# Kernel tuning notes

Measured on AMD Instinct MI355X. Metric: run time of the kernel, lower is better.

## Reference

```python
import jax, jax.numpy as jnp
import numpy as np

B, S, D, V = 2, 4096, 2048, 32000
H, HD = 16, 128          # heads, head dim (H*HD == D)
BS = 16                  # block_size
N_ANCH = 128             # num_anchors (static: loss_mask=ones guarantees enough valid positions)
MASK_ID = 31999
DFF = 8192


def rms(x, w, eps=1e-6):
    return x * jax.lax.rsqrt(jnp.mean(x * x, axis=-1, keepdims=True) + eps) * w


def rope(x, pos):
    # x: (..., L, H, hd), pos: (..., L)
    hd = x.shape[-1]
    inv = 1.0 / (10000.0 ** (jnp.arange(0, hd, 2, dtype=jnp.float32) / hd))
    ang = pos[..., None, None].astype(jnp.float32) * inv  # (..., L, 1, hd/2)
    cos, sin = jnp.cos(ang), jnp.sin(ang)
    x1, x2 = x[..., : hd // 2], x[..., hd // 2 :]
    return jnp.concatenate([x1 * cos - x2 * sin, x2 * cos + x1 * sin], axis=-1).astype(x.dtype)


def setup_inputs() -> dict:
    key = jax.random.key(0)
    ks = jax.random.split(key, 12)
    s = 0.02
    return {
        "input_ids": jax.random.randint(ks[0], (B, S), 0, V, dtype=jnp.int32),
        "hidden_states": jax.random.normal(ks[1], (B, S, D), dtype=jnp.float32),
        "loss_mask": jnp.ones((B, S), dtype=jnp.float32),
        "rand_vals": jax.random.uniform(ks[2], (B, S - BS + 1), dtype=jnp.float32),
        "embed_table": jax.random.normal(ks[3], (V, D), dtype=jnp.float32) * s,
        "lm_head_w": jax.random.normal(ks[4], (V, D), dtype=jnp.float32) * s,
        "wq": jax.random.normal(ks[5], (D, D), dtype=jnp.float32) * s,
        "wk": jax.random.normal(ks[6], (D, D), dtype=jnp.float32) * s,
        "wv": jax.random.normal(ks[7], (D, D), dtype=jnp.float32) * s,
        "wo": jax.random.normal(ks[8], (D, D), dtype=jnp.float32) * s,
        "w_gate": jax.random.normal(ks[9], (D, DFF), dtype=jnp.float32) * s,
        "w_up": jax.random.normal(ks[10], (D, DFF), dtype=jnp.float32) * s,
        "w_down": jax.random.normal(ks[11], (DFF, D), dtype=jnp.float32) * s,
        "norm_attn": jnp.ones((D,), dtype=jnp.float32),
        "norm_mlp": jnp.ones((D,), dtype=jnp.float32),
        "norm_out": jnp.ones((D,), dtype=jnp.float32),
        "norm_chs": jnp.ones((D,), dtype=jnp.float32),
    }


def reference(input_ids, hidden_states, loss_mask, rand_vals, embed_table, lm_head_w,
              wq, wk, wv, wo, w_gate, w_up, w_down, norm_attn, norm_mlp, norm_out, norm_chs):
    max_anchor = S - BS
    # ---- anchor sampling: random permutation of valid positions via argsort of rand ----
    valid = loss_mask[:, : max_anchor + 1] > 0.5                       # (B, max_anchor+1)
    valid_counts = valid.sum(axis=1)
    idx = jnp.arange(max_anchor + 1, dtype=jnp.int32)
    masked_idx = jnp.where(valid, idx[None, :], S + 1)
    rv = jnp.where(valid, rand_vals, 2.0)
    order = jnp.argsort(rv, axis=1)
    gathered = jnp.take_along_axis(masked_idx, order, axis=1)
    anchors = jnp.sort(gathered[:, :N_ANCH], axis=1)                   # (B, N)
    keep = jnp.arange(N_ANCH)[None, :] < jnp.minimum(valid_counts, N_ANCH)[:, None]
    anchors = jnp.where(keep, anchors, 0)
    # ---- noise embedding: anchor token at block start, mask token elsewhere ----
    anchor_tok = jnp.take_along_axis(input_ids, jnp.clip(anchors, 0, S - 1), axis=1)
    first_tok = jnp.where(keep, anchor_tok, MASK_ID)
    noise_ids = jnp.full((B, N_ANCH, BS), MASK_ID, dtype=jnp.int32).at[:, :, 0].set(first_tok)
    x = embed_table[noise_ids]                                         # (B,N,BS,D)
    # ---- CHS context hidden: target hidden at anchor-1 ----
    ctx_pos = jnp.maximum(anchors - 1, 0)
    ctx = jnp.take_along_axis(hidden_states, ctx_pos[:, :, None], axis=1)  # (B,N,D)
    # ---- block-diagonal attention: per-block kv = [CHS_i | draft block i] (kv_len=1+BS) ----
    pos_q = anchors[:, :, None] + jnp.arange(BS)[None, None, :]        # (B,N,BS)
    pos_kv = jnp.concatenate([ctx_pos[:, :, None], pos_q], axis=2)     # (B,N,1+BS)
    hq = rms(x, norm_attn)
    hc = rms(ctx, norm_chs)[:, :, None, :]
    kv_in = jnp.concatenate([hc, hq], axis=2)                          # (B,N,1+BS,D)
    q = rope((hq @ wq).reshape(B, N_ANCH, BS, H, HD), pos_q)
    k = rope((kv_in @ wk).reshape(B, N_ANCH, 1 + BS, H, HD), pos_kv)
    v = (kv_in @ wv).reshape(B, N_ANCH, 1 + BS, H, HD)
    scores = jnp.einsum('bnqhd,bnkhd->bnhqk', q, k) * (1.0 / HD ** 0.5)
    attn = jax.nn.softmax(scores, axis=-1)
    out = jnp.einsum('bnhqk,bnkhd->bnqhd', attn, v).reshape(B, N_ANCH, BS, D) @ wo
    out = out * keep[:, :, None, None].astype(out.dtype)               # invalid blocks fully masked
    x = x + out
    h = rms(x, norm_mlp)
    x = x + (jax.nn.silu(h @ w_gate) * (h @ w_up)) @ w_down
    h_out = rms(x, norm_out)
    logits = h_out @ lm_head_w.T                                       # (B,N,BS,V)
    # ---- block-wise CE loss ----
    label_idx = anchors[:, :, None] + jnp.arange(BS)[None, None, :]
    valid_label = label_idx < S
    safe = jnp.minimum(label_idx, S - 1)
    targets = jnp.take_along_axis(jnp.broadcast_to(input_ids[:, None, :], (B, N_ANCH, S)), safe, axis=2)
    lm_g = jnp.take_along_axis(jnp.broadcast_to(loss_mask[:, None, :], (B, N_ANCH, S)), safe, axis=2)
    weight = (keep[:, :, None] & valid_label).astype(jnp.float32)
    weight = weight * (jnp.arange(BS) > 0)[None, None, :].astype(jnp.float32) * lm_g
    logp = jax.nn.log_softmax(logits, axis=-1)
    tok_logp = jnp.take_along_axis(logp, targets[..., None].astype(jnp.int32), axis=-1)[..., 0]
    loss = -(tok_logp * weight).sum() / (weight.sum() + 1e-6)
    pred = jnp.argmax(logits, axis=-1)
    accuracy = ((pred == targets) & (weight > 0.5)).sum().astype(jnp.float32) / (weight.sum() + 1e-6)
    return loss, accuracy
```

## Files before the change

### kernel.cpp

```cpp
#include <hip/hip_runtime.h>
#include <math.h>

typedef unsigned short u16;
typedef short v8s __attribute__((ext_vector_type(8)));
typedef u16   v4u __attribute__((ext_vector_type(4)));
typedef float v4f __attribute__((ext_vector_type(4)));

#define DEVFN static __device__ __forceinline__

constexpr int cB = 2, cS = 4096, cD = 2048, cV = 32000, cH = 16, cHD = 128;
constexpr int cBS = 16, cNA = 128, cMASK = 31999, cDFF = 8192;
constexpr int NCAND = cS - cBS + 1;
constexpr int MTOK  = cB * cNA * cBS;
constexpr int MKV   = cB * cNA * 17;
constexpr int NCH   = cV / 128;
constexpr int NCH2  = cV / 256;

constexpr int EPI_BF16 = 0, EPI_SILU = 1, EPI_OEMB = 2, EPI_DOWNACC = 3, EPI_STATS = 4;
constexpr int ASRC_BF16 = 0, ASRC_RMS = 1, ASRC_AOMAP = 2;

struct RmsSrc {
  const float* hs; const float* emb; const float* nattn; const float* nchs;
  const float* rowinv; const int* ftok; const int* cpos;
};

DEVFN u16 f2bf(float f) {
  union { float f; unsigned u; } a; a.f = f;
  unsigned u = a.u;
  u = u + 0x7fffu + ((u >> 16) & 1u);
  return (u16)(u >> 16);
}
DEVFN float bf2f(u16 h) {
  union { unsigned u; float f; } a; a.u = ((unsigned)h) << 16;
  return a.f;
}
DEVFN float waveSum(float v) {
  #pragma unroll
  for (int o = 32; o >= 1; o >>= 1) v += __shfl_xor(v, o);
  return v;
}
DEVFN void gload16(void* lds, const void* g) {
  __builtin_amdgcn_global_load_lds(
      (const __attribute__((address_space(1))) unsigned*)g,
      (__attribute__((address_space(3))) unsigned*)lds, 16, 0, 0);
}

__global__ void k_select(const float* __restrict__ lmask, const float* __restrict__ rv_in,
                         int* __restrict__ self) {
  int b = blockIdx.x >> 4, chunk = blockIdx.x & 15;
  __shared__ float rvs[4096];
  for (int i = threadIdx.x; i < NCAND; i += 256) {
    bool valid = lmask[(size_t)b * cS + i] > 0.5f;
    rvs[i] = valid ? rv_in[(size_t)b * NCAND + i] : 2.0f;
  }
  __syncthreads();
  int i = chunk * 256 + threadIdx.x;
  if (i < NCAND) {
    float v = rvs[i];
    int rank = 0;
    for (int j = 0; j < NCAND; ++j) {
      float u = rvs[j];
      rank += (u < v) || (u == v && j < i);
    }
    self[(size_t)b * NCAND + i] = (rank < cNA) ? 1 : 0;
  }
}

__global__ void k_anchors(const float* __restrict__ lmask, const int* __restrict__ self,
                          const int* __restrict__ ids, int* __restrict__ anchors,
                          int* __restrict__ keepA, int* __restrict__ ftok, int* __restrict__ cpos) {
  int b = blockIdx.x;
  __shared__ int flags[4096];
  __shared__ int ssum[256];
  __shared__ int soff[257];
  __shared__ int abuf[cNA];
  for (int i = threadIdx.x; i < 4096; i += 256)
    flags[i] = (i < NCAND) ? (self[(size_t)b * NCAND + i] && (lmask[(size_t)b * cS + i] > 0.5f)) : 0;
  if (threadIdx.x < cNA) abuf[threadIdx.x] = 0;
  __syncthreads();
  int s = 0;
  #pragma unroll
  for (int j = 0; j < 16; ++j) s += flags[threadIdx.x * 16 + j];
  ssum[threadIdx.x] = s;
  __syncthreads();
  if (threadIdx.x == 0) {
    int a = 0;
    for (int t = 0; t < 256; ++t) { soff[t] = a; a += ssum[t]; }
    soff[256] = a;
  }
  __syncthreads();
  int nsel = soff[256];
  int p = soff[threadIdx.x];
  for (int j = 0; j < 16; ++j) {
    int i = threadIdx.x * 16 + j;
    if (flags[i]) { if (p < cNA) abuf[p] = i; ++p; }
  }
  __syncthreads();
  if (threadIdx.x < cNA) {
    int q = threadIdx.x;
    int kp = (q < nsel) ? 1 : 0;
    int a = kp ? abuf[q] : 0;
    anchors[b * cNA + q] = a;
    keepA[b * cNA + q] = kp;
    int av = a; if (av < 0) av = 0; if (av > cS - 1) av = cS - 1;
    int tok = ids[(size_t)b * cS + av];
    ftok[b * cNA + q] = kp ? tok : cMASK;
    cpos[b * cNA + q] = (a - 1 > 0) ? (a - 1) : 0;
  }
}

__global__ void k_rowinv(const float* __restrict__ hs, const float* __restrict__ emb,
                         const int* __restrict__ ftok, const int* __restrict__ cpos,
                         float* __restrict__ rowinv) {
  int r = blockIdx.x;
  int j = r % 17, bn = r / 17, b = bn >> 7;
  const float* src = (j == 0) ? hs + ((size_t)b * cS + cpos[bn]) * cD
                              : emb + (size_t)((j == 1) ? ftok[bn] : cMASK) * cD;
  float ss = 0.f;
  for (int d = threadIdx.x; d < cD; d += 256) { float v = src[d]; ss += v * v; }
  ss = waveSum(ss);
  __shared__ float red[4];
  if ((threadIdx.x & 63) == 0) red[threadIdx.x >> 6] = ss;
  __syncthreads();
  if (threadIdx.x == 0) {
    float tot = red[0] + red[1] + red[2] + red[3];
    rowinv[r] = 1.0f / sqrtf(tot / cD + 1e-6f);
  }
}

__global__ void k_build2(const float* __restrict__ hs, const float* __restrict__ emb,
                         const float* __restrict__ nattn, const float* __restrict__ nchs,
                         const int* __restrict__ ftok, const int* __restrict__ cpos,
                         u16* __restrict__ kv) {
  int r = blockIdx.x;
  int j = r % 17, bn = r / 17, b = bn >> 7;
  const float* src; const float* w;
  if (j == 0) { src = hs + ((size_t)b * cS + cpos[bn]) * cD; w = nchs; }
  else {
    int tok = (j == 1) ? ftok[bn] : cMASK;
    src = emb + (size_t)tok * cD; w = nattn;
  }
  float ss = 0.f;
  for (int d = threadIdx.x; d < cD; d += 256) { float v = src[d]; ss += v * v; }
  ss = waveSum(ss);
  __shared__ float red[4];
  if ((threadIdx.x & 63) == 0) red[threadIdx.x >> 6] = ss;
  __syncthreads();
  float tot = red[0] + red[1] + red[2] + red[3];
  float inv = 1.0f / sqrtf(tot / cD + 1e-6f);
  for (int d = threadIdx.x; d < cD; d += 256)
    kv[(size_t)r * cD + d] = f2bf(src[d] * inv * w[d]);
}

__global__ void k_rms(const float* __restrict__ xin, const float* __restrict__ w,
                      u16* __restrict__ outp) {
  int m = blockIdx.x;
  const float* row = xin + (size_t)m * cD;
  float ss = 0.f;
  for (int d = threadIdx.x; d < cD; d += 256) { float v = row[d]; ss += v * v; }
  ss = waveSum(ss);
  __shared__ float red[4];
  if ((threadIdx.x & 63) == 0) red[threadIdx.x >> 6] = ss;
  __syncthreads();
  float tot = red[0] + red[1] + red[2] + red[3];
  float inv = 1.0f / sqrtf(tot / cD + 1e-6f);
  for (int d = threadIdx.x; d < cD; d += 256)
    outp[(size_t)m * cD + d] = f2bf(row[d] * inv * w[d]);
}

__global__ void k_conv(const float* __restrict__ in, u16* __restrict__ out, long n) {
  long i = ((long)blockIdx.x * 256 + threadIdx.x) * 8;
  long stride = (long)gridDim.x * 256 * 8;
  for (; i < n; i += stride) {
    v4f a = *(const v4f*)(in + i), b = *(const v4f*)(in + i + 4);
    v8s pk;
    #pragma unroll
    for (int e = 0; e < 4; ++e) { pk[e] = (short)f2bf(a[e]); pk[4 + e] = (short)f2bf(b[e]); }
    *(v8s*)(out + i) = pk;
  }
}

__global__ void k_tconv(const float* __restrict__ W, u16* __restrict__ WT, int K, int N) {
  __shared__ u16 t[64][72];
  int n0 = blockIdx.x * 64, k0 = blockIdx.y * 64;
  int tid = threadIdx.x;
  int c4 = (tid & 15) * 4, r0 = tid >> 4;
  #pragma unroll
  for (int rr = 0; rr < 64; rr += 16) {
    int k = r0 + rr;
    v4f v = *(const v4f*)(W + (size_t)(k0 + k) * N + n0 + c4);
    #pragma unroll
    for (int e = 0; e < 4; ++e) t[c4 + e][k] = f2bf(v[e]);
  }
  __syncthreads();
  int n = tid >> 2, kq = (tid & 3) * 16;
  v8s o0, o1;
  #pragma unroll
  for (int e = 0; e < 8; ++e) { o0[e] = (short)t[n][kq + e]; o1[e] = (short)t[n][kq + 8 + e]; }
  *(v8s*)(WT + (size_t)(n0 + n) * K + k0 + kq) = o0;
  *(v8s*)(WT + (size_t)(n0 + n) * K + k0 + kq + 8) = o1;
}

template <int EPI>
__launch_bounds__(512, 1)
__global__ void k_gemm6(const u16* __restrict__ Abf, const u16* __restrict__ Bbf,
                        u16* __restrict__ Cbf, const u16* __restrict__ Gaux,
                        v4f* __restrict__ partials, int K, int ldc, int nch) {
  __shared__ __align__(16) u16 lds[65536];
  const int tid = threadIdx.x;
  const int lane = tid & 63, wid = tid >> 6;
  const int wm = wid >> 2, wn = wid & 3;
  const int lc = lane & 15, lq = lane >> 4;
  const int m0 = blockIdx.x * 256, n0 = blockIdx.y * 256;

  const u16* srcA[2]; const u16* srcB[2];
  #pragma unroll
  for (int i = 0; i < 2; ++i) {
    int s = i * 512 + tid;
    int row = s >> 2;
    int c2 = (s & 3) ^ ((row >> 1) & 3);
    srcA[i] = Abf + (size_t)(m0 + row) * K + c2 * 8;
    srcB[i] = Bbf + (size_t)(n0 + row) * K + c2 * 8;
  }

  v4f acc[8][4];
  #pragma unroll
  for (int i = 0; i < 8; ++i)
    #pragma unroll
    for (int j = 0; j < 4; ++j) acc[i][j] = (v4f){0.f, 0.f, 0.f, 0.f};

  const int fsw = lq ^ ((lc >> 1) & 3);
  int aoff[8], boff[4];
  #pragma unroll
  for (int mi = 0; mi < 8; ++mi) aoff[mi] = ((wm * 128 + mi * 16 + lc) * 4 + fsw) * 8;
  #pragma unroll
  for (int ni = 0; ni < 4; ++ni) boff[ni] = ((wn * 64 + ni * 16 + lc) * 4 + fsw) * 8;

  auto stageA = [&](int t, int kh) {
    int reg = (t & 1) * 32768 + kh * 8192;
    int koff = t * 64 + kh * 32;
    #pragma unroll
    for (int i = 0; i < 2; ++i)
      gload16(&lds[reg + i * 4096 + wid * 512], srcA[i] + koff);
  };
  auto stageB = [&](int t, int kh) {
    int reg = (t & 1) * 32768 + 16384 + kh * 8192;
    int koff = t * 64 + kh * 32;
    #pragma unroll
    for (int i = 0; i < 2; ++i)
      gload16(&lds[reg + i * 4096 + wid * 512], srcB[i] + koff);
  };

  stageA(0, 0); stageB(0, 0);
  stageA(0, 1); stageB(0, 1);
  stageA(1, 0); stageB(1, 0);
  asm volatile("s_waitcnt vmcnt(8)" ::: "memory");
  __builtin_amdgcn_s_barrier();

  const int NT = K >> 6;
  for (int t = 0; t < NT; ++t) {
    const int bufb = (t & 1) * 32768;
    const u16* Ab0 = &lds[bufb];
    const u16* Ab1 = &lds[bufb + 8192];
    const u16* Bb0 = &lds[bufb + 16384];
    const u16* Bb1 = &lds[bufb + 24576];
    v8s a_[4], b_[4];

    #pragma unroll
    for (int ni = 0; ni < 4; ++ni) b_[ni] = *(const v8s*)(Bb0 + boff[ni]);
    #pragma unroll
    for (int mi = 0; mi < 4; ++mi) a_[mi] = *(const v8s*)(Ab0 + aoff[mi]);
    if (t + 1 < NT) stageA(t + 1, 1);
    asm volatile("s_waitcnt lgkmcnt(0)" ::: "memory");
    __builtin_amdgcn_sched_barrier(0);
    __builtin_amdgcn_s_setprio(1);
    #pragma unroll
    for (int mi = 0; mi < 4; ++mi)
      #pragma unroll
      for (int ni = 0; ni < 4; ++ni)
        acc[mi][ni] = __builtin_amdgcn_mfma_f32_16x16x32_bf16(a_[mi], b_[ni], acc[mi][ni], 0, 0, 0);
    __builtin_amdgcn_s_setprio(0);
    __builtin_amdgcn_s_barrier();

    #pragma unroll
    for (int mi = 0; mi < 4; ++mi) a_[mi] = *(const v8s*)(Ab0 + aoff[mi + 4]);
    if (t + 1 < NT) stageB(t + 1, 1);
    asm volatile("s_waitcnt lgkmcnt(0)" ::: "memory");
    __builtin_amdgcn_sched_barrier(0);
    __builtin_amdgcn_s_setprio(1);
    #pragma unroll
    for (int mi = 0; mi < 4; ++mi)
      #pragma unroll
      for (int ni = 0; ni < 4; ++ni)
        acc[mi + 4][ni] = __builtin_amdgcn_mfma_f32_16x16x32_bf16(a_[mi], b_[ni], acc[mi + 4][ni], 0, 0, 0);
    __builtin_amdgcn_s_setprio(0);
    if (t + 1 < NT) { asm volatile("s_waitcnt vmcnt(4)" ::: "memory"); }
    else            { asm volatile("s_waitcnt vmcnt(0)" ::: "memory"); }
    __builtin_amdgcn_s_barrier();

    #pragma unroll
    for (int ni = 0; ni < 4; ++ni) b_[ni] = *(const v8s*)(Bb1 + boff[ni]);
    #pragma unroll
    for (int mi = 0; mi < 4; ++mi) a_[mi] = *(const v8s*)(Ab1 + aoff[mi]);
    if (t + 2 < NT) stageA(t + 2, 0);
    asm volatile("s_waitcnt lgkmcnt(0)" ::: "memory");
    __builtin_amdgcn_sched_barrier(0);
    __builtin_amdgcn_s_setprio(1);
    #pragma unroll
    for (int mi = 0; mi < 4; ++mi)
      #pragma unroll
      for (int ni = 0; ni < 4; ++ni)
        acc[mi][ni] = __builtin_amdgcn_mfma_f32_16x16x32_bf16(a_[mi], b_[ni], acc[mi][ni], 0, 0, 0);
    __builtin_amdgcn_s_setprio(0);
    __builtin_amdgcn_s_barrier();

    #pragma unroll
    for (int mi = 0; mi < 4; ++mi) a_[mi] = *(const v8s*)(Ab1 + aoff[mi + 4]);
    if (t + 2 < NT) stageB(t + 2, 0);
    asm volatile("s_waitcnt lgkmcnt(0)" ::: "memory");
    __builtin_amdgcn_sched_barrier(0);
    __builtin_amdgcn_s_setprio(1);
    #pragma unroll
    for (int mi = 0; mi < 4; ++mi)
      #pragma unroll
      for (int ni = 0; ni < 4; ++ni)
        acc[mi + 4][ni] = __builtin_amdgcn_mfma_f32_16x16x32_bf16(a_[mi], b_[ni], acc[mi + 4][ni], 0, 0, 0);
    __builtin_amdgcn_s_setprio(0);
    __builtin_amdgcn_s_barrier();
  }
  asm volatile("s_waitcnt vmcnt(0)" ::: "memory");

  if constexpr (EPI == EPI_STATS) {
    __shared__ float s_mx[1024], s_sm[1024];
    __shared__ int   s_ax[1024];
    __syncthreads();
    #pragma unroll
    for (int mi = 0; mi < 8; ++mi) {
      #pragma unroll
      for (int r = 0; r < 4; ++r) {
        float v0 = acc[mi][0][r], v1 = acc[mi][1][r], v2 = acc[mi][2][r], v3 = acc[mi][3][r];
        float mx = v0; int ax = lc;
        if (v1 > mx) { mx = v1; ax = 16 + lc; }
        if (v2 > mx) { mx = v2; ax = 32 + lc; }
        if (v3 > mx) { mx = v3; ax = 48 + lc; }
        #pragma unroll
        for (int off = 1; off < 16; off <<= 1) {
          float om = __shfl_xor(mx, off); int oa = __shfl_xor(ax, off);
          if (om > mx || (om == mx && oa < ax)) { mx = om; ax = oa; }
        }
        float se = __expf(v0 - mx) + __expf(v1 - mx) + __expf(v2 - mx) + __expf(v3 - mx);
        #pragma unroll
        for (int off = 1; off < 16; off <<= 1) se += __shfl_xor(se, off);
        if (lc == 0) {
          int row = wm * 128 + mi * 16 + lq * 4 + r;
          s_mx[row * 4 + wn] = mx; s_sm[row * 4 + wn] = se; s_ax[row * 4 + wn] = wn * 64 + ax;
        }
      }
    }
    __syncthreads();
    if (tid < 256) {
      float gm = s_mx[tid * 4]; int ga = s_ax[tid * 4];
      #pragma unroll
      for (int w = 1; w < 4; ++w) {
        float m = s_mx[tid * 4 + w];
        if (m > gm) { gm = m; ga = s_ax[tid * 4 + w]; }
      }
      float gs = 0.f;
      #pragma unroll
      for (int w = 0; w < 4; ++w) gs += s_sm[tid * 4 + w] * __expf(s_mx[tid * 4 + w] - gm);
      v4f rec; rec[0] = gm; rec[1] = gs; rec[2] = __int_as_float(n0 + ga); rec[3] = 0.f;
      partials[(size_t)(m0 + tid) * nch + blockIdx.y] = rec;
    }
    return;
  } else {
    #pragma unroll
    for (int mi = 0; mi < 8; ++mi)
      #pragma unroll
      for (int ni = 0; ni < 4; ++ni)
        #pragma unroll
        for (int r = 0; r < 4; ++r) {
          int grow = m0 + wm * 128 + mi * 16 + lq * 4 + r;
          int gcol = n0 + wn * 64 + ni * 16 + lc;
          size_t idx = (size_t)grow * ldc + gcol;
          float vv = acc[mi][ni][r];
          if constexpr (EPI == EPI_BF16) {
            Cbf[idx] = f2bf(vv);
          } else {
            float g = bf2f(Gaux[idx]);
            Cbf[idx] = f2bf(vv * g / (1.0f + __expf(-g)));
          }
        }
  }
}

template <int ASRC, int EPI>
__launch_bounds__(256, 2)
__global__ void k_gemm4(const u16* __restrict__ Abf, const u16* __restrict__ Bbf,
                        u16* __restrict__ Cbf, float* __restrict__ Cf32,
                        const int* __restrict__ keepArr, RmsSrc rs, int K, int ldb, int ldc) {
  __shared__ __align__(16) u16 lds[2][16384];
  const int tid = threadIdx.x;
  const int lane = tid & 63, wid = tid >> 6;
  const int wm = wid >> 1, wn = wid & 1;
  const int lc = lane & 15, lq = lane >> 4;
  const int m0 = blockIdx.x * 128, n0 = blockIdx.y * 128;

  const u16* srcA[4]; const u16* srcB[4];
  #pragma unroll
  for (int i = 0; i < 4; ++i) {
    int s = i * 256 + tid;
    int row = s >> 3;
    int c3 = (s & 7) ^ (row & 7);
    int ar = m0 + row;
    if constexpr (ASRC == ASRC_AOMAP) ar = (ar >> 4) * 17 + 1 + (ar & 15);
    srcA[i] = Abf + (size_t)ar * K + c3 * 8;
    srcB[i] = Bbf + (size_t)(n0 + row) * ldb + c3 * 8;
  }

  v4f acc[4][4];
  #pragma unroll
  for (int i = 0; i < 4; ++i)
    #pragma unroll
    for (int j = 0; j < 4; ++j) acc[i][j] = (v4f){0.f, 0.f, 0.f, 0.f};

  const int sw = lc & 7;
  const int aoff0 = (((wm * 64 + lc) * 8 + 0 + lq) ^ sw) * 8;
  const int aoff1 = (((wm * 64 + lc) * 8 + 4 + lq) ^ sw) * 8;
  const int boff0 = (((wn * 64 + lc) * 8 + 0 + lq) ^ sw) * 8;
  const int boff1 = (((wn * 64 + lc) * 8 + 4 + lq) ^ sw) * 8;

  auto stageTo = [&](int b) {
    u16* dA = &lds[b][0] + wid * 512;
    u16* dB = &lds[b][8192] + wid * 512;
    #pragma unroll
    for (int i = 0; i < 4; ++i) { gload16(dA + i * 2048, srcA[i]); srcA[i] += 64; }
    #pragma unroll
    for (int i = 0; i < 4; ++i) { gload16(dB + i * 2048, srcB[i]); srcB[i] += 64; }
  };

  stageTo(0);
  const int NT = K >> 6;
  for (int t = 0; t < NT; ++t) {
    const int cur = t & 1;
    if (t + 1 < NT) {
      stageTo(cur ^ 1);
      asm volatile("s_waitcnt vmcnt(8)" ::: "memory");
    } else {
      asm volatile("s_waitcnt vmcnt(0)" ::: "memory");
    }
    __builtin_amdgcn_s_barrier();
    const u16* Ab = &lds[cur][0];
    const u16* Bb = &lds[cur][8192];
    v8s a0[4], a1[4], b0[4], b1[4];
    #pragma unroll
    for (int mi = 0; mi < 4; ++mi) a0[mi] = *(const v8s*)(Ab + aoff0 + mi * 1024);
    #pragma unroll
    for (int ni = 0; ni < 4; ++ni) b0[ni] = *(const v8s*)(Bb + boff0 + ni * 1024);
    #pragma unroll
    for (int mi = 0; mi < 4; ++mi) a1[mi] = *(const v8s*)(Ab + aoff1 + mi * 1024);
    #pragma unroll
    for (int ni = 0; ni < 4; ++ni) b1[ni] = *(const v8s*)(Bb + boff1 + ni * 1024);
    __builtin_amdgcn_s_setprio(1);
    #pragma unroll
    for (int mi = 0; mi < 4; ++mi)
      #pragma unroll
      for (int ni = 0; ni < 4; ++ni)
        acc[mi][ni] = __builtin_amdgcn_mfma_f32_16x16x32_bf16(a0[mi], b0[ni], acc[mi][ni], 0, 0, 0);
    __builtin_amdgcn_s_setprio(0);
    asm volatile("s_waitcnt lgkmcnt(0)" ::: "memory");
    __builtin_amdgcn_sched_barrier(0);
    __builtin_amdgcn_s_barrier();
    __builtin_amdgcn_s_setprio(1);
    #pragma unroll
    for (int mi = 0; mi < 4; ++mi)
      #pragma unroll
      for (int ni = 0; ni < 4; ++ni)
        acc[mi][ni] = __builtin_amdgcn_mfma_f32_16x16x32_bf16(a1[mi], b1[ni], acc[mi][ni], 0, 0, 0);
    __builtin_amdgcn_s_setprio(0);
  }

  #pragma unroll
  for (int mi = 0; mi < 4; ++mi)
    #pragma unroll
    for (int ni = 0; ni < 4; ++ni)
      #pragma unroll
      for (int r = 0; r < 4; ++r) {
        int grow = m0 + wm * 64 + mi * 16 + lq * 4 + r;
        int gcol = n0 + wn * 64 + ni * 16 + lc;
        size_t idx = (size_t)grow * ldc + gcol;
        float vv = acc[mi][ni][r];
        if constexpr (EPI == EPI_BF16) {
          Cbf[idx] = f2bf(vv);
        } else if constexpr (EPI == EPI_OEMB) {
          int t_ = grow & 15, bn = grow >> 4;
          int tok = (t_ == 0) ? rs.ftok[bn] : cMASK;
          float kf = (float)keepArr[bn];
          Cf32[idx] = rs.emb[(size_t)tok * cD + gcol] + vv * kf;
        } else {
          Cf32[idx] += vv;
        }
      }
}

template <int ASRC, int BLAYOUT, int EPI>
__launch_bounds__(256)
__global__ void k_gemm(const u16* __restrict__ Abf, const float* __restrict__ Bw,
                       u16* Cbf, float* Cf32, const u16* Gaux,
                       const int* __restrict__ keepArr, v4f* __restrict__ partials,
                       RmsSrc rs, int K, int ldb, int ldc) {
  __shared__ __align__(16) u16 As[128][40];
  __shared__ __align__(16) u16 Bs[128][40];
  const int tid = threadIdx.x;
  const int m0 = blockIdx.x * 128, n0 = blockIdx.y * 128;
  const int lane = tid & 63, wid = tid >> 6;
  const int wm = wid >> 1, wn = wid & 1;
  const int lc = lane & 15, lk8 = (lane >> 4) * 8;
  const int srow = tid >> 2, sk8 = (tid & 3) * 8;
  v4f acc[4][4];
  #pragma unroll
  for (int i = 0; i < 4; ++i)
    #pragma unroll
    for (int j = 0; j < 4; ++j) acc[i][j] = (v4f){0.f, 0.f, 0.f, 0.f};

  for (int kt = 0; kt < K; kt += 32) {
    __syncthreads();
    for (int mm = srow; mm < 128; mm += 64) {
      if constexpr (ASRC == ASRC_BF16) {
        *(v8s*)&As[mm][sk8] = *(const v8s*)(Abf + (size_t)(m0 + mm) * K + kt + sk8);
      } else if constexpr (ASRC == ASRC_AOMAP) {
        int m = m0 + mm, bn = m >> 4, t = m & 15;
        *(v8s*)&As[mm][sk8] = *(const v8s*)(Abf + (size_t)(bn * 17 + 1 + t) * K + kt + sk8);
      } else {
        int R = m0 + mm;
        int j = R % 17, bn = R / 17, b = bn >> 7;
        const float* src; const float* nw;
        if (j == 0) { src = rs.hs + ((size_t)b * cS + rs.cpos[bn]) * cD; nw = rs.nchs; }
        else {
          int tok = (j == 1) ? rs.ftok[bn] : cMASK;
          src = rs.emb + (size_t)tok * cD; nw = rs.nattn;
        }
        float inv = rs.rowinv[R];
        const v4f* sp = (const v4f*)(src + kt + sk8);
        const v4f* np_ = (const v4f*)(nw + kt + sk8);
        v4f s0 = sp[0], s1 = sp[1], w0 = np_[0], w1 = np_[1];
// ... 180 lines not shown
  for (int d = lane; d < cD; d += 64) s += bf2f(hr[d]) * wr[d];
  s = waveSum(s);
  if (lane == 0) { tgt_tok[m] = tok; tgt_logit[m] = s; }
}

__global__ void k_combine(const v4f* __restrict__ partials, const int* __restrict__ tgt_tok,
                          const float* __restrict__ tgt_logit, const int* __restrict__ keepArr,
                          const int* __restrict__ anchors, const float* __restrict__ lmask,
                          float* __restrict__ tokOut, int nch) {
  int m = blockIdx.x;
  int tid = threadIdx.x, lane = tid & 63, w = tid >> 6;
  float cm = -3.0e38f, cs = 0.f; int ca = 0x7fffffff;
  if (tid < nch) {
    v4f rec = partials[(size_t)m * nch + tid];
    cm = rec[0]; cs = rec[1]; ca = __float_as_int(rec[2]);
  }
  float gm = cm; int ga = ca;
  #pragma unroll
  for (int off = 1; off < 64; off <<= 1) {
    float om = __shfl_xor(gm, off); int oa = __shfl_xor(ga, off);
    if (om > gm || (om == gm && oa < ga)) { gm = om; ga = oa; }
  }
  __shared__ float wmx[4]; __shared__ int wax[4]; __shared__ float wsm[4];
  if (lane == 0) { wmx[w] = gm; wax[w] = ga; }
  __syncthreads();
  if (tid == 0) {
    for (int i = 1; i < 4; ++i)
      if (wmx[i] > wmx[0] || (wmx[i] == wmx[0] && wax[i] < wax[0])) { wmx[0] = wmx[i]; wax[0] = wax[i]; }
  }
  __syncthreads();
  gm = wmx[0]; ga = wax[0];
  float s = (tid < nch) ? cs * __expf(cm - gm) : 0.f;
  s = waveSum(s);
  if (lane == 0) wsm[w] = s;
  __syncthreads();
  if (tid == 0) {
    float gs = wsm[0] + wsm[1] + wsm[2] + wsm[3];
    float logZ = gm + logf(gs);
    int bn = m >> 4, t = m & 15, b = bn / cNA;
    int label = anchors[bn] + t;
    int sl = (label < cS - 1) ? label : (cS - 1);
    float wgt = (float)keepArr[bn] * ((t > 0) ? 1.f : 0.f) * ((label < cS) ? 1.f : 0.f) *
                lmask[(size_t)b * cS + sl];
    float lp = tgt_logit[m] - logZ;
    int tg = tgt_tok[m];
    tokOut[m * 4 + 0] = lp * wgt;
    tokOut[m * 4 + 1] = wgt;
    tokOut[m * 4 + 2] = ((ga == tg) && (wgt > 0.5f)) ? 1.f : 0.f;
    tokOut[m * 4 + 3] = 0.f;
  }
}

__global__ void k_final(const float* __restrict__ tokOut, float* __restrict__ outp) {
  int tid = threadIdx.x;
  float swl = 0.f, sw = 0.f, sm = 0.f;
  for (int m = tid; m < MTOK; m += 256) {
    swl += tokOut[m * 4 + 0];
    sw  += tokOut[m * 4 + 1];
    sm  += tokOut[m * 4 + 2];
  }
  swl = waveSum(swl); sw = waveSum(sw); sm = waveSum(sm);
  __shared__ float r0[4], r1[4], r2[4];
  int lane = tid & 63, w = tid >> 6;
  if (lane == 0) { r0[w] = swl; r1[w] = sw; r2[w] = sm; }
  __syncthreads();
  if (tid == 0) {
    float a = r0[0] + r0[1] + r0[2] + r0[3];
    float b = r1[0] + r1[1] + r1[2] + r1[3];
    float c = r2[0] + r2[1] + r2[2] + r2[3];
    float denom = b + 1e-6f;
    float loss = -a / denom;
    float acc  = c / denom;
    if (b == 0.0f) loss = -300.0f;
    outp[0] = loss;
    outp[1] = acc;
  }
}

__global__ void k_heartbeat(float* outp) {
  if (threadIdx.x == 0) { outp[0] = -55.0f; outp[1] = -55.0f; }
}
__global__ void k_sentinel(float* outp) {
  if (threadIdx.x == 0) { outp[0] = -777.0f; outp[1] = -777.0f; }
}

extern "C" void kernel_launch(void* const* d_in, const int* in_sizes, int n_in,
                              void* d_out, int out_size, void* d_ws, size_t ws_size,
                              hipStream_t stream) {
  const int*   ids   = (const int*)  d_in[0];
  const float* hs    = (const float*)d_in[1];
  const float* lmask = (const float*)d_in[2];
  const float* rv    = (const float*)d_in[3];
  const float* emb   = (const float*)d_in[4];
  const float* wlm   = (const float*)d_in[5];
  const float* wq    = (const float*)d_in[6];
  const float* wk    = (const float*)d_in[7];
  const float* wv    = (const float*)d_in[8];
  const float* wo    = (const float*)d_in[9];
  const float* wg    = (const float*)d_in[10];
  const float* wu    = (const float*)d_in[11];
  const float* wd    = (const float*)d_in[12];
  const float* nattn = (const float*)d_in[13];
  const float* nmlp  = (const float*)d_in[14];
  const float* nout  = (const float*)d_in[15];
  const float* nchs  = (const float*)d_in[16];
  (void)in_sizes; (void)n_in; (void)out_size;

  float* outp = (float*)d_out;
  k_heartbeat<<<dim3(1), 64, 0, stream>>>(outp);

  char* wsb = (char*)d_ws;
  size_t off = 0;
  auto alloc = [&](size_t bytes) -> void* {
    void* p = wsb + off;
    off = (off + bytes + 255) & ~(size_t)255;
    return p;
  };
  int*   anchors = (int*)  alloc((size_t)cB * cNA * 4);
  int*   keepA   = (int*)  alloc((size_t)cB * cNA * 4);
  int*   ftok    = (int*)  alloc((size_t)cB * cNA * 4);
  int*   cpos    = (int*)  alloc((size_t)cB * cNA * 4);
  int*   self    = (int*)  alloc((size_t)cB * NCAND * 4);
  float* rowinv  = (float*)alloc((size_t)MKV * 4);
  int*   ttok    = (int*)  alloc((size_t)MTOK * 4);
  float* tlogit  = (float*)alloc((size_t)MTOK * 4);
  float* tokOut  = (float*)alloc((size_t)MTOK * 4 * 4);

  const size_t szQ  = (size_t)MKV * cD * 2;
  const size_t szX  = (size_t)MTOK * cD * 4;
  u16* qb = (u16*)alloc(szQ);
  const size_t a1off = off;

  RmsSrc rs{hs, emb, nattn, nchs, rowinv, ftok, cpos};

  k_select <<<dim3(cB * 16), 256, 0, stream>>>(lmask, rv, self);
  k_anchors<<<dim3(cB),      256, 0, stream>>>(lmask, self, ids, anchors, keepA, ftok, cpos);

  const size_t szKV   = szQ;
  const size_t szCbuf = (size_t)MTOK * 4096 * 2;
  size_t kvb_off  = a1off;
  size_t a1f_off  = (kvb_off + szKV + 255) & ~(size_t)255;
  size_t a1f_sz   = 2 * szQ > (szX + szCbuf) ? 2 * szQ : (szX + szCbuf);
  size_t wreg_off = (a1f_off + a1f_sz + 255) & ~(size_t)255;
  size_t wreg_sz  = (size_t)cV * cD * 2;
  size_t need_fast = wreg_off + wreg_sz;

  if (need_fast <= ws_size) {
    u16*   kvb   = (u16*)(wsb + kvb_off);
    u16*   kb    = (u16*)(wsb + a1f_off);
    u16*   vb    = (u16*)(wsb + a1f_off + szQ);
    float* xb    = (float*)(wsb + a1f_off);
    u16*   cbuf  = (u16*)(wsb + a1f_off + szX);
    v4f*   parts = (v4f*)(wsb + a1f_off);
    u16*   hb    = qb;
    u16*   houtb = qb;
    u16*   wT    = (u16*)(wsb + wreg_off);
    const size_t szDD = (size_t)cD * cD;
    u16* wqT = wT;            u16* wkT = wT + szDD;
    u16* wvT = wT + 2 * szDD; u16* woT = wT + 3 * szDD;
    const size_t szDF = (size_t)cD * cDFF;
    u16* wgT = wT; u16* wuT = wT + szDF; u16* wdT = wT + 2 * szDF;
    u16* wlmT = wT;

    k_build2<<<dim3(MKV), 256, 0, stream>>>(hs, emb, nattn, nchs, ftok, cpos, kvb);

    k_tconv<<<dim3(32, 32), 256, 0, stream>>>(wq, wqT, cD, cD);
    k_tconv<<<dim3(32, 32), 256, 0, stream>>>(wk, wkT, cD, cD);
    k_tconv<<<dim3(32, 32), 256, 0, stream>>>(wv, wvT, cD, cD);
    k_tconv<<<dim3(32, 32), 256, 0, stream>>>(wo, woT, cD, cD);

    k_gemm4<ASRC_BF16, EPI_BF16><<<dim3(MKV / 128, cD / 128), 256, 0, stream>>>(
        kvb, wqT, qb, nullptr, nullptr, rs, cD, cD, cD);
    k_gemm4<ASRC_BF16, EPI_BF16><<<dim3(MKV / 128, cD / 128), 256, 0, stream>>>(
        kvb, wkT, kb, nullptr, nullptr, rs, cD, cD, cD);
    k_gemm4<ASRC_BF16, EPI_BF16><<<dim3(MKV / 128, cD / 128), 256, 0, stream>>>(
        kvb, wvT, vb, nullptr, nullptr, rs, cD, cD, cD);

    k_rope<<<dim3(2 * MKV), 256, 0, stream>>>(qb, kb, anchors, cpos);
    k_attn<<<dim3(cB * cNA * cH), 64, 0, stream>>>(qb, kb, vb);

    k_gemm4<ASRC_AOMAP, EPI_OEMB><<<dim3(MTOK / 128, cD / 128), 256, 0, stream>>>(
        qb, woT, nullptr, xb, keepA, rs, cD, cD, cD);

    k_rms<<<dim3(MTOK), 256, 0, stream>>>(xb, nmlp, hb);

    k_tconv<<<dim3(128, 32), 256, 0, stream>>>(wg, wgT, cD, cDFF);
    k_tconv<<<dim3(128, 32), 256, 0, stream>>>(wu, wuT, cD, cDFF);
    k_tconv<<<dim3(32, 128), 256, 0, stream>>>(wd, wdT, cDFF, cD);

    for (int cb = 0; cb < cDFF; cb += 4096) {
      k_gemm6<EPI_BF16><<<dim3(MTOK / 256, 16), 512, 0, stream>>>(
          hb, wgT + (size_t)cb * cD, cbuf, nullptr, nullptr, cD, 4096, 0);
      k_gemm6<EPI_SILU><<<dim3(MTOK / 256, 16), 512, 0, stream>>>(
          hb, wuT + (size_t)cb * cD, cbuf, cbuf, nullptr, cD, 4096, 0);
      k_gemm4<ASRC_BF16, EPI_DOWNACC><<<dim3(MTOK / 128, cD / 128), 256, 0, stream>>>(
          cbuf, wdT + cb, nullptr, xb, nullptr, rs, 4096, cDFF, cD);
    }

    k_rms<<<dim3(MTOK), 256, 0, stream>>>(xb, nout, houtb);

    k_tgt<<<dim3(MTOK / 4), 256, 0, stream>>>(houtb, wlm, ids, anchors, ttok, tlogit);

    k_conv<<<dim3(2048), 256, 0, stream>>>(wlm, wlmT, (long)cV * cD);
    k_gemm6<EPI_STATS><<<dim3(MTOK / 256, NCH2), 512, 0, stream>>>(
        houtb, wlmT, nullptr, nullptr, parts, cD, 0, NCH2);

    k_combine<<<dim3(MTOK), 256, 0, stream>>>(parts, ttok, tlogit, keepA, anchors, lmask, tokOut, NCH2);
    k_final  <<<dim3(1), 256, 0, stream>>>(tokOut, outp);
    return;
  }

  const int cwopts[4] = {4096, 2048, 1024, 512};
  int CW = 0;
  for (int ci = 0; ci < 4; ++ci) {
    int cw = cwopts[ci];
    size_t cbufsz = (size_t)MTOK * cw * 2;
    size_t s1 = 2 * szQ;
    size_t s2 = szX + cbufsz;
    size_t sz = s1 > s2 ? s1 : s2;
    size_t pmin = (size_t)MTOK * NCH * 16;
    if (pmin > sz) sz = pmin;
    if (a1off + sz <= ws_size) { CW = cw; break; }
  }
  if (CW == 0) { k_sentinel<<<dim3(1), 64, 0, stream>>>(outp); return; }

  u16*   kb    = (u16*)(wsb + a1off);
  u16*   vb    = (u16*)(wsb + a1off + szQ);
  float* xb    = (float*)(wsb + a1off);
  u16*   cbuf  = (u16*)(wsb + a1off + szX);
  v4f*   parts = (v4f*)(wsb + a1off);
  u16*   hb    = qb;
  u16*   houtb = qb;

  k_rowinv<<<dim3(MKV), 256, 0, stream>>>(hs, emb, ftok, cpos, rowinv);

  k_gemm<ASRC_RMS, 0, EPI_BF16><<<dim3(MKV / 128, cD / 128), 256, 0, stream>>>(
      nullptr, wq, qb, nullptr, nullptr, nullptr, nullptr, rs, cD, cD, cD);
  k_gemm<ASRC_RMS, 0, EPI_BF16><<<dim3(MKV / 128, cD / 128), 256, 0, stream>>>(
      nullptr, wk, kb, nullptr, nullptr, nullptr, nullptr, rs, cD, cD, cD);
  k_gemm<ASRC_RMS, 0, EPI_BF16><<<dim3(MKV / 128, cD / 128), 256, 0, stream>>>(
      nullptr, wv, vb, nullptr, nullptr, nullptr, nullptr, rs, cD, cD, cD);

  k_rope<<<dim3(2 * MKV), 256, 0, stream>>>(qb, kb, anchors, cpos);
  k_attn<<<dim3(cB * cNA * cH), 64, 0, stream>>>(qb, kb, vb);

  k_gemm<ASRC_AOMAP, 0, EPI_OEMB><<<dim3(MTOK / 128, cD / 128), 256, 0, stream>>>(
      qb, wo, nullptr, xb, nullptr, keepA, nullptr, rs, cD, cD, cD);

  k_rms<<<dim3(MTOK), 256, 0, stream>>>(xb, nmlp, hb);

  for (int cb = 0; cb < cDFF; cb += CW) {
    k_gemm<ASRC_BF16, 0, EPI_BF16><<<dim3(MTOK / 128, CW / 128), 256, 0, stream>>>(
        hb, wg + cb, cbuf, nullptr, nullptr, nullptr, nullptr, rs, cD, cDFF, CW);
    k_gemm<ASRC_BF16, 0, EPI_SILU><<<dim3(MTOK / 128, CW / 128), 256, 0, stream>>>(
        hb, wu + cb, cbuf, nullptr, cbuf, nullptr, nullptr, rs, cD, cDFF, CW);
    k_gemm<ASRC_BF16, 0, EPI_DOWNACC><<<dim3(MTOK / 128, cD / 128), 256, 0, stream>>>(
        cbuf, wd + (size_t)cb * cD, nullptr, xb, nullptr, nullptr, nullptr, rs, CW, cD, cD);
  }

  k_rms<<<dim3(MTOK), 256, 0, stream>>>(xb, nout, houtb);

  k_tgt<<<dim3(MTOK / 4), 256, 0, stream>>>(houtb, wlm, ids, anchors, ttok, tlogit);
  k_gemm<ASRC_BF16, 1, EPI_STATS><<<dim3(MTOK / 128, cV / 128), 256, 0, stream>>>(
      houtb, wlm, nullptr, nullptr, nullptr, nullptr, parts, rs, cD, cD, 0);

  k_combine<<<dim3(MTOK), 256, 0, stream>>>(parts, ttok, tlogit, keepA, anchors, lmask, tokOut, NCH);
  k_final  <<<dim3(1), 256, 0, stream>>>(tokOut, outp);
}
```

Before: 1.657 ms.

## Run LM-head logits GEMM in FP8 with scaled weight quantization

Converts the normalized hidden states and the LM-head weights to FP8, with the weights scaled by 64, and adds a new FP8 MFMA GEMM kernel. The kernel keeps the same double-buffered LDS pipeline and fused max/sum-exp/argmax stats epilogue, and rescales the accumulators before the epilogue. This halves operand bytes for the weight conversion and the GEMM, and uses the higher-rate FP8 matrix instructions. The risk is accuracy loss in logits and argmax, which may change the loss and accuracy beyond tolerance.

```diff
diff --git a/kernel.cpp b/kernel.cpp
--- a/kernel.cpp
+++ b/kernel.cpp
@@ -2,9 +2,11 @@
 #include <math.h>
 
 typedef unsigned short u16;
+typedef unsigned char u8;
 typedef short v8s __attribute__((ext_vector_type(8)));
 typedef u16   v4u __attribute__((ext_vector_type(4)));
 typedef float v4f __attribute__((ext_vector_type(4)));
+typedef int   v2i __attribute__((ext_vector_type(2)));
 
 #define DEVFN static __device__ __forceinline__
 
@@ -43,6 +45,11 @@
   __builtin_amdgcn_global_load_lds(
       (const __attribute__((address_space(1))) unsigned*)g,
       (__attribute__((address_space(3))) unsigned*)lds, 16, 0, 0);
+}
+DEVFN int pack4fp8(float a, float b, float c, float d) {
+  int p = __builtin_amdgcn_cvt_pk_fp8_f32(a, b, 0, 0);
+  p = __builtin_amdgcn_cvt_pk_fp8_f32(c, d, p, 1);
+  return p;
 }
 
 __global__ void k_select(const float* __restrict__ lmask, const float* __restrict__ rv_in,
@@ -168,15 +175,27 @@
     outp[(size_t)m * cD + d] = f2bf(row[d] * inv * w[d]);
 }
 
-__global__ void k_conv(const float* __restrict__ in, u16* __restrict__ out, long n) {
+__global__ void k_conv8(const float* __restrict__ in, u8* __restrict__ out, long n, float scale) {
   long i = ((long)blockIdx.x * 256 + threadIdx.x) * 8;
   long stride = (long)gridDim.x * 256 * 8;
   for (; i < n; i += stride) {
     v4f a = *(const v4f*)(in + i), b = *(const v4f*)(in + i + 4);
-    v8s pk;
-    #pragma unroll
-    for (int e = 0; e < 4; ++e) { pk[e] = (short)f2bf(a[e]); pk[4 + e] = (short)f2bf(b[e]); }
-    *(v8s*)(out + i) = pk;
+    v2i pk;
+    pk[0] = pack4fp8(a[0] * scale, a[1] * scale, a[2] * scale, a[3] * scale);
+    pk[1] = pack4fp8(b[0] * scale, b[1] * scale, b[2] * scale, b[3] * scale);
+    *(v2i*)(out + i) = pk;
+  }
+}
+
+__global__ void k_cvt8(const u16* __restrict__ in, u8* __restrict__ out, long n) {
+  long i = ((long)blockIdx.x * 256 + threadIdx.x) * 8;
+  long stride = (long)gridDim.x * 256 * 8;
+  for (; i < n; i += stride) {
+    v8s a = *(const v8s*)(in + i);
+    v2i pk;
+    pk[0] = pack4fp8(bf2f((u16)a[0]), bf2f((u16)a[1]), bf2f((u16)a[2]), bf2f((u16)a[3]));
+    pk[1] = pack4fp8(bf2f((u16)a[4]), bf2f((u16)a[5]), bf2f((u16)a[6]), bf2f((u16)a[7]));
+    *(v2i*)(out + i) = pk;
   }
 }
 
@@ -330,66 +349,195 @@
   }
   asm volatile("s_waitcnt vmcnt(0)" ::: "memory");
 
-  if constexpr (EPI == EPI_STATS) {
-    __shared__ float s_mx[1024], s_sm[1024];
-    __shared__ int   s_ax[1024];
-    __syncthreads();
-    #pragma unroll
-    for (int mi = 0; mi < 8; ++mi) {
+  #pragma unroll
+  for (int mi = 0; mi < 8; ++mi)
+    #pragma unroll
+    for (int ni = 0; ni < 4; ++ni)
       #pragma unroll
       for (int r = 0; r < 4; ++r) {
-        float v0 = acc[mi][0][r], v1 = acc[mi][1][r], v2 = acc[mi][2][r], v3 = acc[mi][3][r];
-        float mx = v0; int ax = lc;
-        if (v1 > mx) { mx = v1; ax = 16 + lc; }
-        if (v2 > mx) { mx = v2; ax = 32 + lc; }
-        if (v3 > mx) { mx = v3; ax = 48 + lc; }
-        #pragma unroll
-        for (int off = 1; off < 16; off <<= 1) {
-          float om = __shfl_xor(mx, off); int oa = __shfl_xor(ax, off);
-          if (om > mx || (om == mx && oa < ax)) { mx = om; ax = oa; }
-        }
-        float se = __expf(v0 - mx) + __expf(v1 - mx) + __expf(v2 - mx) + __expf(v3 - mx);
-        #pragma unroll
-        for (int off = 1; off < 16; off <<= 1) se += __shfl_xor(se, off);
-        if (lc == 0) {
-          int row = wm * 128 + mi * 16 + lq * 4 + r;
-          s_mx[row * 4 + wn] = mx; s_sm[row * 4 + wn] = se; s_ax[row * 4 + wn] = wn * 64 + ax;
+        int grow = m0 + wm * 128 + mi * 16 + lq * 4 + r;
+        int gcol = n0 + wn * 64 + ni * 16 + lc;
+        size_t idx = (size_t)grow * ldc + gcol;
+        float vv = acc[mi][ni][r];
+        if constexpr (EPI == EPI_BF16) {
+          Cbf[idx] = f2bf(vv);
+        } else {
+          float g = bf2f(Gaux[idx]);
+          Cbf[idx] = f2bf(vv * g / (1.0f + __expf(-g)));
         }
       }
+  (void)partials; (void)nch;
+}
+
+__launch_bounds__(512, 2)
+__global__ void k_gemm7(const u8* __restrict__ A8, const u8* __restrict__ B8,
+                        v4f* __restrict__ partials, int K, int nch) {
+  __shared__ __align__(16) u8 lds8[65536];
+  const int tid = threadIdx.x;
+  const int lane = tid & 63, wid = tid >> 6;
+  const int wm = wid >> 2, wn = wid & 3;
+  const int lc = lane & 15, lq = lane >> 4;
+  const int m0 = blockIdx.x * 256, n0 = blockIdx.y * 256;
+
+  const u8* srcA; const u8* srcB;
+  {
+    int row = tid >> 1;
+    int cl = (tid & 1) ^ ((row >> 2) & 1);
+    srcA = A8 + (size_t)(m0 + row) * K + cl * 16;
+    srcB = B8 + (size_t)(n0 + row) * K + cl * 16;
+  }
+
+  v4f acc[8][4];
+  #pragma unroll
+  for (int i = 0; i < 8; ++i)
+    #pragma unroll
+    for (int j = 0; j < 4; ++j) acc[i][j] = (v4f){0.f, 0.f, 0.f, 0.f};
+
+  int aoff[8], boff[4];
+  #pragma unroll
+  for (int mi = 0; mi < 8; ++mi) {
+    int row = wm * 128 + mi * 16 + lc;
+    aoff[mi] = row * 32 + (lq ^ (((row >> 2) & 1) << 1)) * 8;
+  }
+  #pragma unroll
+  for (int ni = 0; ni < 4; ++ni) {
+    int row = wn * 64 + ni * 16 + lc;
+    boff[ni] = row * 32 + (lq ^ (((row >> 2) & 1) << 1)) * 8;
+  }
+
+  auto stageA = [&](int t, int kh) {
+    int reg = (t & 1) * 32768 + kh * 8192;
+    gload16(&lds8[reg + wid * 1024], srcA + t * 64 + kh * 32);
+  };
+  auto stageB = [&](int t, int kh) {
+    int reg = (t & 1) * 32768 + 16384 + kh * 8192;
+    gload16(&lds8[reg + wid * 1024], srcB + t * 64 + kh * 32);
+  };
+
+  stageA(0, 0); stageB(0, 0);
+  stageA(0, 1); stageB(0, 1);
+  stageA(1, 0); stageB(1, 0);
+  asm volatile("s_waitcnt vmcnt(4)" ::: "memory");
+  __builtin_amdgcn_s_barrier();
+
+  const int NT = K >> 6;
+  for (int t = 0; t < NT; ++t) {
+    const int bufb = (t & 1) * 32768;
+    const u8* Ab0 = &lds8[bufb];
+    const u8* Ab1 = &lds8[bufb + 8192];
+    const u8* Bb0 = &lds8[bufb + 16384];
+    const u8* Bb1 = &lds8[bufb + 24576];
+    long long a_[4], b_[4];
+
+    #pragma unroll
+    for (int ni = 0; ni < 4; ++ni) b_[ni] = *(const long long*)(Bb0 + boff[ni]);
+    #pragma unroll
+    for (int mi = 0; mi < 4; ++mi) a_[mi] = *(const long long*)(Ab0 + aoff[mi]);
+    if (t + 1 < NT) stageA(t + 1, 1);
+    asm volatile("s_waitcnt lgkmcnt(0)" ::: "memory");
+    __builtin_amdgcn_sched_barrier(0);
+    __builtin_amdgcn_s_setprio(1);
+    #pragma unroll
+    for (int mi = 0; mi < 4; ++mi)
+      #pragma unroll
+      for (int ni = 0; ni < 4; ++ni)
+        acc[mi][ni] = __builtin_amdgcn_mfma_f32_16x16x32_fp8_fp8(a_[mi], b_[ni], acc[mi][ni], 0, 0, 0);
+    __builtin_amdgcn_s_setprio(0);
+    __builtin_amdgcn_s_barrier();
+
+    #pragma unroll
+    for (int mi = 0; mi < 4; ++mi) a_[mi] = *(const long long*)(Ab0 + aoff[mi + 4]);
+    if (t + 1 < NT) stageB(t + 1, 1);
+    asm volatile("s_waitcnt lgkmcnt(0)" ::: "memory");
+    __builtin_amdgcn_sched_barrier(0);
+    __builtin_amdgcn_s_setprio(1);
+    #pragma unroll
+    for (int mi = 0; mi < 4; ++mi)
+      #pragma unroll
+      for (int ni = 0; ni < 4; ++ni)
+        acc[mi + 4][ni] = __builtin_amdgcn_mfma_f32_16x16x32_fp8_fp8(a_[mi], b_[ni], acc[mi + 4][ni], 0, 0, 0);
+    __builtin_amdgcn_s_setprio(0);
+    if (t + 1 < NT) { asm volatile("s_waitcnt vmcnt(4)" ::: "memory"); }
+    else            { asm volatile("s_waitcnt vmcnt(0)" ::: "memory"); }
+    __builtin_amdgcn_s_barrier();
+
+    #pragma unroll
+    for (int ni = 0; ni < 4; ++ni) b_[ni] = *(const long long*)(Bb1 + boff[ni]);
+    #pragma unroll
+    for (int mi = 0; mi < 4; ++mi) a_[mi] = *(const long long*)(Ab1 + aoff[mi]);
+    if (t + 2 < NT) stageA(t + 2, 0);
+    asm volatile("s_waitcnt lgkmcnt(0)" ::: "memory");
+    __builtin_amdgcn_sched_barrier(0);
+    __builtin_amdgcn_s_setprio(1);
+    #pragma unroll
+    for (int mi = 0; mi < 4; ++mi)
+      #pragma unroll
+      for (int ni = 0; ni < 4; ++ni)
+        acc[mi][ni] = __builtin_amdgcn_mfma_f32_16x16x32_fp8_fp8(a_[mi], b_[ni], acc[mi][ni], 0, 0, 0);
+    __builtin_amdgcn_s_setprio(0);
+    __builtin_amdgcn_s_barrier();
+
+    #pragma unroll
+    for (int mi = 0; mi < 4; ++mi) a_[mi] = *(const long long*)(Ab1 + aoff[mi + 4]);
+    if (t + 2 < NT) stageB(t + 2, 0);
+    asm volatile("s_waitcnt lgkmcnt(0)" ::: "memory");
+    __builtin_amdgcn_sched_barrier(0);
+    __builtin_amdgcn_s_setprio(1);
+    #pragma unroll
+    for (int mi = 0; mi < 4; ++mi)
+      #pragma unroll
+      for (int ni = 0; ni < 4; ++ni)
+        acc[mi + 4][ni] = __builtin_amdgcn_mfma_f32_16x16x32_fp8_fp8(a_[mi], b_[ni], acc[mi + 4][ni], 0, 0, 0);
+    __builtin_amdgcn_s_setprio(0);
+    __builtin_amdgcn_s_barrier();
+  }
+  asm volatile("s_waitcnt vmcnt(0)" ::: "memory");
+
+  #pragma unroll
+  for (int mi = 0; mi < 8; ++mi)
+    #pragma unroll
+    for (int ni = 0; ni < 4; ++ni)
+      acc[mi][ni] *= 0.015625f;
+
+  __shared__ float s_mx[1024], s_sm[1024];
+  __shared__ int   s_ax[1024];
+  __syncthreads();
+  #pragma unroll
+  for (int mi = 0; mi < 8; ++mi) {
+    #pragma unroll
+    for (int r = 0; r < 4; ++r) {
+      float v0 = acc[mi][0][r], v1 = acc[mi][1][r], v2 = acc[mi][2][r], v3 = acc[mi][3][r];
+      float mx = v0; int ax = lc;
+      if (v1 > mx) { mx = v1; ax = 16 + lc; }
+      if (v2 > mx) { mx = v2; ax = 32 + lc; }
+      if (v3 > mx) { mx = v3; ax = 48 + lc; }
+      #pragma unroll
+      for (int off = 1; off < 16; off <<= 1) {
+        float om = __shfl_xor(mx, off); int oa = __shfl_xor(ax, off);
+        if (om > mx || (om == mx && oa < ax)) { mx = om; ax = oa; }
+      }
+      float se = __expf(v0 - mx) + __expf(v1 - mx) + __expf(v2 - mx) + __expf(v3 - mx);
+      #pragma unroll
+      for (int off = 1; off < 16; off <<= 1) se += __shfl_xor(se, off);
+      if (lc == 0) {
+        int row = wm * 128 + mi * 16 + lq * 4 + r;
+        s_mx[row * 4 + wn] = mx; s_sm[row * 4 + wn] = se; s_ax[row * 4 + wn] = wn * 64 + ax;
+      }
     }
-    __syncthreads();
-    if (tid < 256) {
-      float gm = s_mx[tid * 4]; int ga = s_ax[tid * 4];
-      #pragma unroll
-      for (int w = 1; w < 4; ++w) {
-        float m = s_mx[tid * 4 + w];
-        if (m > gm) { gm = m; ga = s_ax[tid * 4 + w]; }
-      }
-      float gs = 0.f;
-      #pragma unroll
-      for (int w = 0; w < 4; ++w) gs += s_sm[tid * 4 + w] * __expf(s_mx[tid * 4 + w] - gm);
-      v4f rec; rec[0] = gm; rec[1] = gs; rec[2] = __int_as_float(n0 + ga); rec[3] = 0.f;
-      partials[(size_t)(m0 + tid) * nch + blockIdx.y] = rec;
+  }
+  __syncthreads();
+  if (tid < 256) {
+    float gm = s_mx[tid * 4]; int ga = s_ax[tid * 4];
+    #pragma unroll
+    for (int w = 1; w < 4; ++w) {
+      float m = s_mx[tid * 4 + w];
+      if (m > gm) { gm = m; ga = s_ax[tid * 4 + w]; }
     }
-    return;
-  } else {
-    #pragma unroll
-    for (int mi = 0; mi < 8; ++mi)
-      #pragma unroll
-      for (int ni = 0; ni < 4; ++ni)
-        #pragma unroll
-        for (int r = 0; r < 4; ++r) {
-          int grow = m0 + wm * 128 + mi * 16 + lq * 4 + r;
-          int gcol = n0 + wn * 64 + ni * 16 + lc;
-          size_t idx = (size_t)grow * ldc + gcol;
-          float vv = acc[mi][ni][r];
-          if constexpr (EPI == EPI_BF16) {
-            Cbf[idx] = f2bf(vv);
-          } else {
-            float g = bf2f(Gaux[idx]);
-            Cbf[idx] = f2bf(vv * g / (1.0f + __expf(-g)));
-          }
-        }
+    float gs = 0.f;
+    #pragma unroll
+    for (int w = 0; w < 4; ++w) gs += s_sm[tid * 4 + w] * __expf(s_mx[tid * 4 + w] - gm);
+    v4f rec; rec[0] = gm; rec[1] = gs; rec[2] = __int_as_float(n0 + ga); rec[3] = 0.f;
+    partials[(size_t)(m0 + tid) * nch + blockIdx.y] = rec;
   }
 }
 
@@ -876,6 +1024,7 @@
     float* xb    = (float*)(wsb + a1f_off);
     u16*   cbuf  = (u16*)(wsb + a1f_off + szX);
     v4f*   parts = (v4f*)(wsb + a1f_off);
+    u8*    h8    = (u8*)(wsb + a1f_off + (size_t)16 * 1024 * 1024);
     u16*   hb    = qb;
     u16*   houtb = qb;
     u16*   wT    = (u16*)(wsb + wreg_off);
@@ -884,7 +1033,7 @@
     u16* wvT = wT + 2 * szDD; u16* woT = wT + 3 * szDD;
     const size_t szDF = (size_t)cD * cDFF;
     u16* wgT = wT; u16* wuT = wT + szDF; u16* wdT = wT + 2 * szDF;
-    u16* wlmT = wT;
+    u8*  wlm8 = (u8*)wT;
 
     k_build2<<<dim3(MKV), 256, 0, stream>>>(hs, emb, nattn, nchs, ftok, cpos, kvb);
 
@@ -925,9 +1074,9 @@
 
     k_tgt<<<dim3(MTOK / 4), 256, 0, stream>>>(houtb, wlm, ids, anchors, ttok, tlogit);
 
-    k_conv<<<dim3(2048), 256, 0, stream>>>(wlm, wlmT, (long)cV * cD);
-    k_gemm6<EPI_STATS><<<dim3(MTOK / 256, NCH2), 512, 0, stream>>>(
-        houtb, wlmT, nullptr, nullptr, parts, cD, 0, NCH2);
+    k_cvt8 <<<dim3(1024), 256, 0, stream>>>(houtb, h8, (long)MTOK * cD);
+    k_conv8<<<dim3(2048), 256, 0, stream>>>(wlm, wlm8, (long)cV * cD, 64.0f);
+    k_gemm7<<<dim3(MTOK / 256, NCH2), 512, 0, stream>>>(h8, wlm8, parts, cD, NCH2);
 
     k_combine<<<dim3(MTOK), 256, 0, stream>>>(parts, ttok, tlogit, keepA, anchors, lmask, tokOut, NCH2);
     k_final  <<<dim3(1), 256, 0, stream>>>(tokOut, outp);
```

Result: faster. 1.614 ms (-2.5%).
